# Optimization experiments

Hardware: AMD Instinct MI355X
Metric: run time of the kernel (lower is better)

Reference implementation:

```python
import jax, jax.numpy as jnp
import numpy as np

DIM = 128
NUM_HEADS = 4
WS = 7          # window_size
SHIFT = 3       # shift_size
H = W = 56
B = 64
SCALE = DIM ** (-0.5)  # note: module scales by dim**-0.5, not head_dim**-0.5
NEG_INF = -1e9


def _make_attn_mask():
    # Static Swin shifted-window mask, built with numpy at trace time.
    img = np.zeros((H, W), dtype=np.float32)
    slices = (slice(0, -WS), slice(-WS, -SHIFT), slice(-SHIFT, None))
    cnt = 0
    for hs in slices:
        for ws_ in slices:
            img[hs, ws_] = cnt
            cnt += 1
    # window partition: [nW, WS*WS]
    m = img.reshape(H // WS, WS, W // WS, WS).transpose(0, 2, 1, 3).reshape(-1, WS * WS)
    am = m[:, None, :] - m[:, :, None]          # [nW, N, N]
    am = np.where(am != 0, NEG_INF, 0.0).astype(np.float32)
    return jnp.asarray(am)


def _window_partition(x):
    # x: [B, H, W, C] -> [B*nW, WS*WS, C]
    Bx, Hx, Wx, C = x.shape
    x = x.reshape(Bx, Hx // WS, WS, Wx // WS, WS, C)
    x = x.transpose(0, 1, 3, 2, 4, 5)
    return x.reshape(-1, WS * WS, C)


def _window_reverse(w):
    # w: [B*nW, WS*WS, C] -> [B, H, W, C]
    C = w.shape[-1]
    x = w.reshape(B, H // WS, W // WS, WS, WS, C)
    x = x.transpose(0, 1, 3, 2, 4, 5)
    return x.reshape(B, H, W, C)


def setup_inputs() -> dict:
    key = jax.random.key(0)
    k1, k2, k3 = jax.random.split(key, 3)
    x = jax.random.normal(k1, (B, H, W, DIM), dtype=jnp.float32)
    qkv_w = jax.random.normal(k2, (DIM, 3 * DIM), dtype=jnp.float32) * 0.02
    qkv_b = jnp.zeros((3 * DIM,), dtype=jnp.float32)
    proj_w = jax.random.normal(k3, (DIM, DIM), dtype=jnp.float32) * 0.02
    proj_b = jnp.zeros((DIM,), dtype=jnp.float32)
    return {"x": x, "qkv_w": qkv_w, "qkv_b": qkv_b, "proj_w": proj_w, "proj_b": proj_b}


def reference(x, qkv_w, qkv_b, proj_w, proj_b):
    attn_mask = _make_attn_mask()                       # [nW, N, N]
    N = WS * WS
    hd = DIM // NUM_HEADS

    shifted = jnp.roll(x, shift=(-SHIFT, -SHIFT), axis=(1, 2))
    xw = _window_partition(shifted)                     # [B*nW, N, C]

    qkv = xw @ qkv_w + qkv_b                            # [B*nW, N, 3C]
    qkv = qkv.reshape(-1, N, 3, NUM_HEADS, hd)
    q, k, v = qkv[:, :, 0], qkv[:, :, 1], qkv[:, :, 2]  # [B*nW, N, h, hd]

    attn = jnp.einsum('wnhd,wmhd->whnm', q, k) * SCALE  # [B*nW, h, N, N]
    nW = attn_mask.shape[0]
    attn = attn.reshape(B, nW, NUM_HEADS, N, N) + attn_mask[None, :, None, :, :]
    attn = jax.nn.softmax(attn.reshape(-1, NUM_HEADS, N, N), axis=-1)

    out = jnp.einsum('whnm,wmhd->wnhd', attn, v).reshape(-1, N, DIM)
    out = out @ proj_w + proj_b                         # [B*nW, N, C]

    shifted_out = _window_reverse(out)                  # [B, H, W, C]
    return jnp.roll(shifted_out, shift=(SHIFT, SHIFT), axis=(1, 2))
```

## Files before the change

### kernel.cpp

```cpp
#include <hip/hip_runtime.h>
#include <hip/hip_bf16.h>


#define NTOK 49
#define QS (0.08838834764831844f * 1.4426950408889634f)

typedef __bf16 bf16x8 __attribute__((ext_vector_type(8)));
typedef __bf16 bf16x2 __attribute__((ext_vector_type(2)));
typedef float  f32x4  __attribute__((ext_vector_type(4)));
typedef unsigned int u32x4 __attribute__((ext_vector_type(4)));

__device__ __forceinline__ f32x4 mfma_bf16(bf16x8 a, bf16x8 b, f32x4 c) {
  return __builtin_amdgcn_mfma_f32_16x16x32_bf16(a, b, c, 0, 0, 0);
}

__device__ __forceinline__ unsigned int pack2(float lo, float hi) {
  bf16x2 t; t[0] = (__bf16)lo; t[1] = (__bf16)hi;
  return __builtin_bit_cast(unsigned int, t);
}

__device__ __forceinline__ bf16x8 cvt8(f32x4 a, f32x4 b) {
  bf16x8 r;
#pragma unroll
  for (int j = 0; j < 4; ++j) { r[j] = (__bf16)a[j]; r[4 + j] = (__bf16)b[j]; }
  return r;
}

__device__ __forceinline__ int regid(int t, int wh, int ww) {
  int i = t / 7;
  int j = t - i * 7;
  int rh = (wh == 7) ? ((i < 4) ? 1 : 2) : 0;
  int rw = (ww == 7) ? ((j < 4) ? 1 : 2) : 0;
  return rh * 3 + rw;
}

__global__ void repack_w(const float* __restrict__ w, ushort* __restrict__ packed,
                         int ncol, int scale_below, float scale) {
  int ctg  = blockIdx.x;
  int kt   = threadIdx.x >> 6;
  int lane = threadIdx.x & 63;
  int col  = ctg * 16 + (lane & 15);
  int k0   = kt * 32 + (lane >> 4) * 8;
  float s  = (ctg < scale_below) ? scale : 1.0f;
  ushort* dst = packed + (size_t)((ctg * 4 + kt) * 64 + lane) * 8;
#pragma unroll
  for (int j = 0; j < 8; ++j) {
    __bf16 h = (__bf16)(w[(size_t)(k0 + j) * ncol + col] * s);
    dst[j] = __builtin_bit_cast(ushort, h);
  }
}

__global__ __launch_bounds__(256, 3)
void swin_fused(const float* __restrict__ x,
                const float* __restrict__ qkv_b,
                const float* __restrict__ proj_b,
                const ushort* __restrict__ pqkv,
                const ushort* __restrict__ pproj,
                float* __restrict__ out)
{
  __shared__ alignas(16) ushort ao[64 * 136];

  const int wid = blockIdx.x;
  const int b   = wid >> 6;
  const int wh  = (wid >> 3) & 7;
  const int ww  = wid & 7;
  const int tid  = threadIdx.x;
  const int wave = tid >> 6;
  const int lane = tid & 63;
  const int c    = lane & 15;
  const int g    = lane >> 4;
  const f32x4 zf = {0.f, 0.f, 0.f, 0.f};

  bf16x8 xf[4][4];
#pragma unroll
  for (int nt = 0; nt < 4; ++nt) {
    int token = nt * 16 + c;
    bool valid = token < NTOK;
    int tc = valid ? token : 0;
    int i = tc / 7;
    int j = tc - i * 7;
    int gh = wh * 7 + i + 3; if (gh >= 56) gh -= 56;
    int gw = ww * 7 + j + 3; if (gw >= 56) gw -= 56;
    const float* src = x + (((size_t)((b * 56 + gh) * 56 + gw)) << 7) + g * 8;
#pragma unroll
    for (int kt = 0; kt < 4; ++kt) {
      f32x4 lo = *reinterpret_cast<const f32x4*>(src + kt * 32);
      f32x4 hi = *reinterpret_cast<const f32x4*>(src + kt * 32 + 4);
      bf16x8 v = cvt8(lo, hi);
      xf[nt][kt] = valid ? v : bf16x8{};
    }
  }

  bf16x8 kf[4], qf[4], vf[2][2];

#pragma unroll
  for (int o = 0; o < 2; ++o) {
    f32x4 qc[2][4];
#pragma unroll
    for (int mt = 0; mt < 2; ++mt)
#pragma unroll
      for (int nt = 0; nt < 4; ++nt) qc[mt][nt] = zf;
#pragma unroll
    for (int kt = 0; kt < 4; ++kt) {
      bf16x8 w0 = *reinterpret_cast<const bf16x8*>(
          pqkv + (size_t)((((o ? 0 : 8) + wave * 2 + 0) * 4 + kt) * 64 + lane) * 8);
      bf16x8 w1 = *reinterpret_cast<const bf16x8*>(
          pqkv + (size_t)((((o ? 0 : 8) + wave * 2 + 1) * 4 + kt) * 64 + lane) * 8);
#pragma unroll
      for (int nt = 0; nt < 4; ++nt) {
        qc[0][nt] = mfma_bf16(w0, xf[nt][kt], qc[0][nt]);
        qc[1][nt] = mfma_bf16(w1, xf[nt][kt], qc[1][nt]);
      }
    }
    float bscale = o ? QS : 1.0f;
    int bbase = (o ? 0 : 128) + wave * 32;
#pragma unroll
    for (int mt = 0; mt < 2; ++mt)
#pragma unroll
      for (int r = 0; r < 4; ++r) {
        float bv = qkv_b[bbase + mt * 16 + g * 4 + r] * bscale;
#pragma unroll
        for (int nt = 0; nt < 4; ++nt) qc[mt][nt][r] += bv;
      }
#pragma unroll
    for (int t = 0; t < 4; ++t) {
      u32x4 u;
      u[0] = pack2(qc[0][t][0], qc[0][t][1]);
      u[1] = pack2(qc[0][t][2], qc[0][t][3]);
      u[2] = pack2(qc[1][t][0], qc[1][t][1]);
      u[3] = pack2(qc[1][t][2], qc[1][t][3]);
      if (o) qf[t] = __builtin_bit_cast(bf16x8, u);
      else   kf[t] = __builtin_bit_cast(bf16x8, u);
    }
  }

  {
    f32x4 vc[4][2];
#pragma unroll
    for (int mt = 0; mt < 4; ++mt) { vc[mt][0] = zf; vc[mt][1] = zf; }
#pragma unroll
    for (int kt = 0; kt < 4; ++kt) {
      bf16x8 w0 = *reinterpret_cast<const bf16x8*>(
          pqkv + (size_t)(((16 + wave * 2 + 0) * 4 + kt) * 64 + lane) * 8);
      bf16x8 w1 = *reinterpret_cast<const bf16x8*>(
          pqkv + (size_t)(((16 + wave * 2 + 1) * 4 + kt) * 64 + lane) * 8);
#pragma unroll
      for (int mt = 0; mt < 4; ++mt) {
        vc[mt][0] = mfma_bf16(xf[mt][kt], w0, vc[mt][0]);
        vc[mt][1] = mfma_bf16(xf[mt][kt], w1, vc[mt][1]);
      }
    }
    float bv0 = qkv_b[256 + wave * 32 + c];
    float bv1 = qkv_b[256 + wave * 32 + 16 + c];
#pragma unroll
    for (int mt = 0; mt < 4; ++mt)
#pragma unroll
      for (int r = 0; r < 4; ++r) { vc[mt][0][r] += bv0; vc[mt][1][r] += bv1; }
#pragma unroll
    for (int kt = 0; kt < 2; ++kt)
#pragma unroll
      for (int nv = 0; nv < 2; ++nv) {
        u32x4 u;
        u[0] = pack2(vc[2 * kt][nv][0], vc[2 * kt][nv][1]);
        u[1] = pack2(vc[2 * kt][nv][2], vc[2 * kt][nv][3]);
        u[2] = pack2(vc[2 * kt + 1][nv][0], vc[2 * kt + 1][nv][1]);
        u[3] = pack2(vc[2 * kt + 1][nv][2], vc[2 * kt + 1][nv][3]);
        vf[kt][nv] = __builtin_bit_cast(bf16x8, u);
      }
  }

  bf16x8 mk[4];
#pragma unroll
  for (int t = 0; t < 4; ++t) {
    int tok = t * 16 + c;
    int rk = (tok < NTOK) ? regid(tok, wh, ww) : 99;
    int d = rk - g * 4;
    unsigned long long mm =
        ((unsigned)d < 4u) ? (0x4180ull << (d * 16)) : 0ull;
    u32x4 u = {(unsigned int)mm, (unsigned int)(mm >> 32), 0u, 0u};
    mk[t] = __builtin_bit_cast(bf16x8, u);
  }

  bf16x8 ppf[2][4];
  float rinv[4];
#pragma unroll
  for (int n = 0; n < 4; ++n) {
    f32x4 stn[4];
#pragma unroll
    for (int m = 0; m < 4; ++m) {
      stn[m] = mfma_bf16(mk[m], mk[n], zf);
      stn[m] = mfma_bf16(kf[m], qf[n], stn[m]);
    }
    float mx = -1e30f;
#pragma unroll
    for (int m = 0; m < 4; ++m)
#pragma unroll
      for (int r = 0; r < 4; ++r) mx = fmaxf(mx, stn[m][r]);
    mx = fmaxf(mx, __shfl_xor(mx, 16));
    mx = fmaxf(mx, __shfl_xor(mx, 32));
    float e[4][4];
    float sm = 0.f;
#pragma unroll
    for (int m = 0; m < 4; ++m)
#pragma unroll
      for (int r = 0; r < 4; ++r) {
        float ev = exp2f(stn[m][r] - mx);
        e[m][r] = ev;
        sm += ev;
      }
    sm += __shfl_xor(sm, 16);
    sm += __shfl_xor(sm, 32);
    rinv[n] = __fdividef(1.f, sm);
#pragma unroll
    for (int kt = 0; kt < 2; ++kt) {
      u32x4 u;
      u[0] = pack2(e[2 * kt][0], e[2 * kt][1]);
      u[1] = pack2(e[2 * kt][2], e[2 * kt][3]);
      u[2] = pack2(e[2 * kt + 1][0], e[2 * kt + 1][1]);
      u[3] = pack2(e[2 * kt + 1][2], e[2 * kt + 1][3]);
      ppf[kt][n] = __builtin_bit_cast(bf16x8, u);
    }
  }

#pragma unroll
  for (int nv = 0; nv < 2; ++nv)
#pragma unroll
    for (int n = 0; n < 4; ++n) {
      f32x4 po = mfma_bf16(vf[0][nv], ppf[0][n], zf);
      po = mfma_bf16(vf[1][nv], ppf[1][n], po);
      float ri = rinv[n];
      uint2 w;
      w.x = pack2(po[0] * ri, po[1] * ri);
      w.y = pack2(po[2] * ri, po[3] * ri);
      *reinterpret_cast<uint2*>(
          &ao[(n * 16 + c) * 136 + wave * 32 + nv * 16 + g * 4]) = w;
    }
  __syncthreads();

  f32x4 acc2[4][2];
#pragma unroll
  for (int m = 0; m < 4; ++m) { acc2[m][0] = zf; acc2[m][1] = zf; }
#pragma unroll
  for (int kt = 0; kt < 4; ++kt) {
    bf16x8 b20 = *reinterpret_cast<const bf16x8*>(
        pproj + (size_t)(((wave * 2 + 0) * 4 + kt) * 64 + lane) * 8);
    bf16x8 b21 = *reinterpret_cast<const bf16x8*>(
        pproj + (size_t)(((wave * 2 + 1) * 4 + kt) * 64 + lane) * 8);
#pragma unroll
    for (int m = 0; m < 4; ++m) {
      bf16x8 af = *reinterpret_cast<const bf16x8*>(&ao[(m * 16 + c) * 136 + kt * 32 + g * 8]);
      acc2[m][0] = mfma_bf16(af, b20, acc2[m][0]);
      acc2[m][1] = mfma_bf16(af, b21, acc2[m][1]);
    }
  }
  float pb0 = proj_b[wave * 32 + c];
  float pb1 = proj_b[wave * 32 + 16 + c];

#pragma unroll
  for (int m = 0; m < 4; ++m)
#pragma unroll
    for (int r = 0; r < 4; ++r) {
      int token = m * 16 + g * 4 + r;
      if (token < NTOK) {
        int i = token / 7;
        int j = token - i * 7;
        int oh = wh * 7 + i + 3; if (oh >= 56) oh -= 56;
        int ow = ww * 7 + j + 3; if (ow >= 56) ow -= 56;
        float* dst = out + (((size_t)((b * 56 + oh) * 56 + ow)) << 7) + wave * 32;
        dst[c]      = acc2[m][0][r] + pb0;
        dst[16 + c] = acc2[m][1][r] + pb1;
      }
    }
}

extern "C" void kernel_launch(void* const* d_in, const int* in_sizes, int n_in,
                              void* d_out, int out_size, void* d_ws, size_t ws_size,
                              hipStream_t stream) {
  const float* x      = (const float*)d_in[0];
  const float* qkv_w  = (const float*)d_in[1];
  const float* qkv_b  = (const float*)d_in[2];
  const float* proj_w = (const float*)d_in[3];
  const float* proj_b = (const float*)d_in[4];
  float* out = (float*)d_out;

  ushort* pqkv  = (ushort*)d_ws;
  ushort* pproj = pqkv + 49152;

  repack_w<<<24, 256, 0, stream>>>(qkv_w, pqkv, 384, 8, QS);
  repack_w<<<8, 256, 0, stream>>>(proj_w, pproj, 128, 0, 1.0f);
  swin_fused<<<4096, 256, 0, stream>>>(x, qkv_b, proj_b, pqkv, pproj, out);
}
```

Baseline: 270.5 us.

## Stage window input in swizzled LDS instead of per-wave register copies

Previously every wave loaded and converted the whole 64x128 window input into 16 bf16x8 registers, so each block read it four times. Now the block loads it cooperatively once into a swizzled LDS buffer that shares storage with the attention-output buffer. Each MFMA reads its operand from LDS, which frees registers and lets launch bounds ask for 4 blocks per SIMD instead of 3. The cost is two extra barriers and LDS read traffic inside the QKV loops.

```diff
diff --git a/kernel.cpp b/kernel.cpp
--- a/kernel.cpp
+++ b/kernel.cpp
@@ -32,6 +32,12 @@
   int rh = (wh == 7) ? ((i < 4) ? 1 : 2) : 0;
   int rw = (ww == 7) ? ((j < 4) ? 1 : 2) : 0;
   return rh * 3 + rw;
+}
+
+__device__ __forceinline__ int xaddr(int tok, int chunk) {
+  int cell = chunk * 64 + tok;
+  int sw = (((tok >> 3) ^ chunk) & 3) << 4;
+  return (cell * 8) ^ sw;
 }
 
 __global__ void repack_w(const float* __restrict__ w, ushort* __restrict__ packed,
@@ -50,7 +56,7 @@
   }
 }
 
-__global__ __launch_bounds__(256, 3)
+__global__ __launch_bounds__(256, 4)
 void swin_fused(const float* __restrict__ x,
                 const float* __restrict__ qkv_b,
                 const float* __restrict__ proj_b,
@@ -58,7 +64,9 @@
                 const ushort* __restrict__ pproj,
                 float* __restrict__ out)
 {
-  __shared__ alignas(16) ushort ao[64 * 136];
+  __shared__ alignas(16) ushort lds[8704];
+  ushort* const xs = lds;
+  ushort* const ao = lds;
 
   const int wid = blockIdx.x;
   const int b   = wid >> 6;
@@ -71,25 +79,27 @@
   const int g    = lane >> 4;
   const f32x4 zf = {0.f, 0.f, 0.f, 0.f};
 
-  bf16x8 xf[4][4];
-#pragma unroll
-  for (int nt = 0; nt < 4; ++nt) {
-    int token = nt * 16 + c;
-    bool valid = token < NTOK;
-    int tc = valid ? token : 0;
-    int i = tc / 7;
-    int j = tc - i * 7;
-    int gh = wh * 7 + i + 3; if (gh >= 56) gh -= 56;
-    int gw = ww * 7 + j + 3; if (gw >= 56) gw -= 56;
-    const float* src = x + (((size_t)((b * 56 + gh) * 56 + gw)) << 7) + g * 8;
-#pragma unroll
-    for (int kt = 0; kt < 4; ++kt) {
-      f32x4 lo = *reinterpret_cast<const f32x4*>(src + kt * 32);
-      f32x4 hi = *reinterpret_cast<const f32x4*>(src + kt * 32 + 4);
+  {
+    int chunk = tid & 15;
+    int tokb  = tid >> 4;
+#pragma unroll
+    for (int it = 0; it < 4; ++it) {
+      int tok = tokb + it * 16;
+      bool valid = tok < NTOK;
+      int tc = valid ? tok : 0;
+      int ti = tc / 7;
+      int tj = tc - ti * 7;
+      int gh = wh * 7 + ti + 3; if (gh >= 56) gh -= 56;
+      int gw = ww * 7 + tj + 3; if (gw >= 56) gw -= 56;
+      const float* src = x + (((size_t)((b * 56 + gh) * 56 + gw)) << 7) + chunk * 8;
+      f32x4 lo = *reinterpret_cast<const f32x4*>(src);
+      f32x4 hi = *reinterpret_cast<const f32x4*>(src + 4);
       bf16x8 v = cvt8(lo, hi);
-      xf[nt][kt] = valid ? v : bf16x8{};
-    }
-  }
+      if (!valid) v = bf16x8{};
+      *reinterpret_cast<bf16x8*>(&xs[xaddr(tok, chunk)]) = v;
+    }
+  }
+  __syncthreads();
 
   bf16x8 kf[4], qf[4], vf[2][2];
 
@@ -108,8 +118,9 @@
           pqkv + (size_t)((((o ? 0 : 8) + wave * 2 + 1) * 4 + kt) * 64 + lane) * 8);
 #pragma unroll
       for (int nt = 0; nt < 4; ++nt) {
-        qc[0][nt] = mfma_bf16(w0, xf[nt][kt], qc[0][nt]);
-        qc[1][nt] = mfma_bf16(w1, xf[nt][kt], qc[1][nt]);
+        bf16x8 xn = *reinterpret_cast<const bf16x8*>(&xs[xaddr(nt * 16 + c, kt * 4 + g)]);
+        qc[0][nt] = mfma_bf16(w0, xn, qc[0][nt]);
+        qc[1][nt] = mfma_bf16(w1, xn, qc[1][nt]);
       }
     }
     float bscale = o ? QS : 1.0f;
@@ -146,8 +157,9 @@
           pqkv + (size_t)(((16 + wave * 2 + 1) * 4 + kt) * 64 + lane) * 8);
 #pragma unroll
       for (int mt = 0; mt < 4; ++mt) {
-        vc[mt][0] = mfma_bf16(xf[mt][kt], w0, vc[mt][0]);
-        vc[mt][1] = mfma_bf16(xf[mt][kt], w1, vc[mt][1]);
+        bf16x8 xn = *reinterpret_cast<const bf16x8*>(&xs[xaddr(mt * 16 + c, kt * 4 + g)]);
+        vc[mt][0] = mfma_bf16(xn, w0, vc[mt][0]);
+        vc[mt][1] = mfma_bf16(xn, w1, vc[mt][1]);
       }
     }
     float bv0 = qkv_b[256 + wave * 32 + c];
@@ -168,6 +180,7 @@
         vf[kt][nv] = __builtin_bit_cast(bf16x8, u);
       }
   }
+  __syncthreads();
 
   bf16x8 mk[4];
 #pragma unroll
```

Measured after the change: 245.5 us. 9.2% less time.
